# Kernel optimization log

Measured on AMD Instinct MI355X. Metric: run time of the kernel, lower is better.

## Reference

```python
import jax, jax.numpy as jnp
import numpy as np

N_NODES = 50000
N_EDGES = 600000
EMB_DIM = 128
HIDDEN = 128
BN_EPS = 1e-5


def setup_inputs() -> dict:
    key = jax.random.key(0)
    ks = jax.random.split(key, 8)
    s_in = 1.0 / np.sqrt(EMB_DIM)
    s_h = 1.0 / np.sqrt(HIDDEN)
    return {
        "x_idx": jnp.arange(N_NODES, dtype=jnp.int32),
        "edge_index": jax.random.randint(ks[0], (2, N_EDGES), 0, N_NODES, dtype=jnp.int32),
        "emb_table": jax.random.normal(ks[1], (N_NODES, EMB_DIM), jnp.float32),
        # ClusterGCNConv: lin_out (bias=False) and lin_root (bias=False)
        "W_out": jax.random.uniform(ks[2], (HIDDEN, EMB_DIM), jnp.float32, -s_in, s_in),
        "W_root": jax.random.uniform(ks[3], (HIDDEN, EMB_DIM), jnp.float32, -s_in, s_in),
        "bn0_gamma": jnp.ones((HIDDEN,), jnp.float32),
        "bn0_beta": jnp.zeros((HIDDEN,), jnp.float32),
        # SGConv 1 (K=1, add_self_loops=True, Linear with bias)
        "W_sg1": jax.random.uniform(ks[4], (HIDDEN, HIDDEN), jnp.float32, -s_h, s_h),
        "b_sg1": jnp.zeros((HIDDEN,), jnp.float32),
        "bn1_gamma": jnp.ones((HIDDEN,), jnp.float32),
        "bn1_beta": jnp.zeros((HIDDEN,), jnp.float32),
        # SGConv 2 (final layer)
        "W_sg2": jax.random.uniform(ks[5], (HIDDEN, HIDDEN), jnp.float32, -s_h, s_h),
        "b_sg2": jnp.zeros((HIDDEN,), jnp.float32),
    }


def _cluster_gcn(x, row, col, W_out, W_root, n):
    # PyG ClusterGCNConv (add_self_loops=False, diag_lambda=0, bias=False):
    # out[c] = sum_{(r->c)} (1/deg(c)) * x[r];  return out @ W_out^T + x @ W_root^T
    deg = jax.ops.segment_sum(jnp.ones_like(col, dtype=x.dtype), col, num_segments=n)
    deg_inv = 1.0 / jnp.maximum(deg, 1.0)
    msg = x[row] * deg_inv[col][:, None]                  # [E, D]
    agg = jax.ops.segment_sum(msg, col, num_segments=n)   # [N, D]
    return agg @ W_out.T + x @ W_root.T


def _sg_conv(x, row, col, W, b, n):
    # PyG SGConv K=1 with gcn_norm: A_hat = D^{-1/2}(A+I)D^{-1/2}, then Linear.
    loop = jnp.arange(n, dtype=row.dtype)
    r = jnp.concatenate([row, loop])
    c = jnp.concatenate([col, loop])
    deg = jax.ops.segment_sum(jnp.ones_like(c, dtype=x.dtype), c, num_segments=n)
    dis = jnp.where(deg > 0, jax.lax.rsqrt(jnp.maximum(deg, 1e-12)), 0.0)
    ew = dis[r] * dis[c]                                   # [E+N]
    agg = jax.ops.segment_sum(x[r] * ew[:, None], c, num_segments=n)
    return agg @ W.T + b


def _bn(x, gamma, beta):
    # BatchNorm1d in training mode: batch statistics, biased variance.
    mu = x.mean(axis=0)
    var = ((x - mu) ** 2).mean(axis=0)
    return (x - mu) * jax.lax.rsqrt(var + BN_EPS) * gamma + beta


def reference(x_idx, edge_index, emb_table, W_out, W_root, bn0_gamma, bn0_beta,
              W_sg1, b_sg1, bn1_gamma, bn1_beta, W_sg2, b_sg2):
    n = emb_table.shape[0]
    row, col = edge_index[0], edge_index[1]
    x = emb_table[x_idx]                                   # [N, D]
    # layer 0: ClusterGCNConv -> BN -> ReLU (dropout p=0)
    x = _cluster_gcn(x, row, col, W_out, W_root, n)
    x = jax.nn.relu(_bn(x, bn0_gamma, bn0_beta))
    # layer 1: SGConv -> BN -> ReLU
    x = _sg_conv(x, row, col, W_sg1, b_sg1, n)
    x = jax.nn.relu(_bn(x, bn1_gamma, bn1_beta))
    # final SGConv
    return _sg_conv(x, row, col, W_sg2, b_sg2, n)
```

## Files before the change

### kernel.cpp

```cpp
#include <hip/hip_runtime.h>
#include <stdint.h>

#define NN 50000
#define NE 600000
#define DD 128
#define BN_EPS 1e-5f

typedef __attribute__((ext_vector_type(8))) short short8;
typedef __attribute__((ext_vector_type(4))) float f32x4;

__device__ __forceinline__ float bf2f(uint16_t u) {
    union { uint32_t u; float f; } v; v.u = ((uint32_t)u) << 16; return v.f;
}
__device__ __forceinline__ uint16_t f2bf(float f) {
    union { float f; uint32_t u; } v; v.f = f;
    return (uint16_t)((v.u + 0x7FFFu + ((v.u >> 16) & 1u)) >> 16);
}
__device__ __forceinline__ float lo16(uint32_t v) { return bf2f((uint16_t)(v & 0xFFFFu)); }
__device__ __forceinline__ float hi16(uint32_t v) { return bf2f((uint16_t)(v >> 16)); }

__global__ void k_count(const int* __restrict__ col, int* __restrict__ cnt) {
    int e = blockIdx.x * 256 + threadIdx.x;
    if (e < NE) atomicAdd(&cnt[col[e]], 1);
}

__global__ void k_alloc(const int* __restrict__ cnt, int* __restrict__ cursor,
                        int* __restrict__ off, int* __restrict__ fillp,
                        float* __restrict__ deginv, float* __restrict__ dis,
                        int* __restrict__ csr_row) {
    int i = blockIdx.x * 256 + threadIdx.x;
    if (i >= NN) return;
    int deg = cnt[i];
    int padded = (deg + 7) & ~7;
    int base = atomicAdd(cursor, padded);
    off[i] = base;
    fillp[i] = base;
    deginv[i] = 1.0f / fmaxf((float)deg, 1.0f);
    dis[i] = rsqrtf((float)deg + 1.0f);
    for (int p = deg; p < padded; ++p) csr_row[base + p] = NN;
}

__global__ void k_fill(const int* __restrict__ ei, int* __restrict__ fillp,
                       int* __restrict__ csr_row) {
    int e = blockIdx.x * 256 + threadIdx.x;
    if (e < NE) {
        int c = ei[NE + e];
        int p = atomicAdd(&fillp[c], 1);
        csr_row[p] = ei[e];
    }
}

__global__ void k_gather(const int* __restrict__ x_idx, const float* __restrict__ emb,
                         uint16_t* __restrict__ xb) {
    int idx = blockIdx.x * 256 + threadIdx.x;
    if (idx >= (NN + 1) * 32) return;
    int node = idx >> 5, c4 = (idx & 31) << 2;
    ushort4 o;
    if (node == NN) {
        o.x = 0; o.y = 0; o.z = 0; o.w = 0;
    } else {
        int src = x_idx[node];
        float4 v = *(const float4*)(emb + (size_t)src * DD + c4);
        o.x = f2bf(v.x); o.y = f2bf(v.y); o.z = f2bf(v.z); o.w = f2bf(v.w);
    }
    *(ushort4*)(xb + (size_t)node * DD + c4) = o;
}

template<int MODE>
__global__ __launch_bounds__(256)
void k_agg(const uint16_t* __restrict__ xb, const int* __restrict__ off,
           const int* __restrict__ cnt, const int* __restrict__ csr_row,
           const float* __restrict__ deginv, const float* __restrict__ dis,
           uint16_t* __restrict__ aggb) {
    int node = blockIdx.x * 4 + (threadIdx.x >> 6);
    if (node >= NN) return;
    int lane = threadIdx.x & 63;
    const uint32_t* __restrict__ xw = (const uint32_t*)xb;
    float a0 = 0.0f, a1 = 0.0f;
    if (MODE == 1) {
        uint32_t v = xw[(size_t)node * 64 + lane];
        a0 = lo16(v); a1 = hi16(v);
    }
    int s = off[node];
    int padded = (cnt[node] + 7) & ~7;
    for (int base = 0; base < padded; base += 64) {
        int rem = min(padded - base, 64);
        int idxv = (lane < rem) ? csr_row[s + base + lane] : NN;
        for (int i = 0; i < rem; i += 8) {
            uint32_t v[8];
            #pragma unroll
            for (int u = 0; u < 8; ++u) {
                int r = __builtin_amdgcn_readlane(idxv, i + u);
                v[u] = xw[(size_t)r * 64 + lane];
            }
            #pragma unroll
            for (int u = 0; u < 8; ++u) { a0 += lo16(v[u]); a1 += hi16(v[u]); }
        }
    }
    float sc = (MODE == 1) ? dis[node] : deginv[node];
    a0 *= sc; a1 *= sc;
    uint32_t o = (uint32_t)f2bf(a0) | ((uint32_t)f2bf(a1) << 16);
    *(uint32_t*)(aggb + (size_t)node * DD + lane * 2) = o;
}

template<bool DUAL, bool STATS, bool BIAS, bool STORE_BF16>
__global__ __launch_bounds__(256, 2)
void k_gemm(const uint16_t* __restrict__ A1, const uint16_t* __restrict__ A2,
            const float* __restrict__ W1, const float* __restrict__ W2,
            const float* __restrict__ bias, float* __restrict__ Hf,
            uint16_t* __restrict__ Hb, float* __restrict__ stats) {
    __shared__ uint16_t Alds[128 * 128];
    __shared__ uint16_t Wlds[128 * 128];
    const int t = threadIdx.x;
    const int lane = t & 63, wid = t >> 6;
    const int wm = (wid >> 1) * 64, wn = (wid & 1) * 64;
    const int m0 = blockIdx.x * 128;
    f32x4 zero = {0.0f, 0.0f, 0.0f, 0.0f};
    f32x4 acc[4][4];
    #pragma unroll
    for (int m = 0; m < 4; ++m)
        #pragma unroll
        for (int n = 0; n < 4; ++n) acc[m][n] = zero;

    const int NP = DUAL ? 2 : 1;
    for (int p = 0; p < NP; ++p) {
        const uint16_t* A = (DUAL && p) ? A2 : A1;
        const float* W = (DUAL && p) ? W2 : W1;
        if (p) __syncthreads();
        #pragma unroll
        for (int it = 0; it < 8; ++it) {
            int idx = it * 256 + t;
            int row = idx >> 4, c16 = idx & 15;
            uint32_t boff = (uint32_t)(row * 256 + ((c16 * 16) ^ ((row & 7) << 4)));
            uint4 v = make_uint4(0u, 0u, 0u, 0u);
            if (m0 + row < NN)
                v = *(const uint4*)(A + (size_t)(m0 + row) * DD + c16 * 8);
            *(uint4*)((char*)Alds + boff) = v;
        }
        #pragma unroll
        for (int it = 0; it < 8; ++it) {
            int idx = it * 256 + t;
            int row = idx >> 4, c8 = idx & 15;
            const float* wp = W + row * DD + c8 * 8;
            float4 v0 = *(const float4*)(wp);
            float4 v1 = *(const float4*)(wp + 4);
            uint4 pk;
            pk.x = (uint32_t)f2bf(v0.x) | ((uint32_t)f2bf(v0.y) << 16);
            pk.y = (uint32_t)f2bf(v0.z) | ((uint32_t)f2bf(v0.w) << 16);
            pk.z = (uint32_t)f2bf(v1.x) | ((uint32_t)f2bf(v1.y) << 16);
            pk.w = (uint32_t)f2bf(v1.z) | ((uint32_t)f2bf(v1.w) << 16);
            uint32_t boff = (uint32_t)(row * 256 + ((c8 * 16) ^ ((row & 7) << 4)));
            *(uint4*)((char*)Wlds + boff) = pk;
        }
        __syncthreads();
        #pragma unroll
        for (int ks = 0; ks < 4; ++ks) {
            short8 a[4], b[4];
            int kb = ks * 64 + ((lane >> 4) << 4);
            #pragma unroll
            for (int m = 0; m < 4; ++m) {
                int row = wm + m * 16 + (lane & 15);
                a[m] = *(const short8*)((const char*)Alds + row * 256 + (kb ^ ((row & 7) << 4)));
            }
            #pragma unroll
            for (int n = 0; n < 4; ++n) {
                int row = wn + n * 16 + (lane & 15);
                b[n] = *(const short8*)((const char*)Wlds + row * 256 + (kb ^ ((row & 7) << 4)));
            }
            #pragma unroll
            for (int m = 0; m < 4; ++m)
                #pragma unroll
                for (int n = 0; n < 4; ++n)
                    acc[m][n] = __builtin_amdgcn_mfma_f32_16x16x32_bf16(a[m], b[n], acc[m][n], 0, 0, 0);
        }
    }
    #pragma unroll
    for (int n = 0; n < 4; ++n) {
        int col = wn + n * 16 + (lane & 15);
        float bb = BIAS ? bias[col] : 0.0f;
        float ssum = 0.0f, ssq = 0.0f;
        #pragma unroll
        for (int m = 0; m < 4; ++m) {
            int rbase = m0 + wm + m * 16 + ((lane >> 4) << 2);
            #pragma unroll
            for (int i = 0; i < 4; ++i) {
                int gr = rbase + i;
                if (gr < NN) {
                    float v = acc[m][n][i] + bb;
                    if (STORE_BF16) Hb[(size_t)gr * DD + col] = f2bf(v);
                    else            Hf[(size_t)gr * DD + col] = v;
                    ssum += v; ssq += v * v;
                }
            }
        }
        if (STATS) {
            ssum += __shfl_xor(ssum, 16, 64);
            ssum += __shfl_xor(ssum, 32, 64);
            ssq  += __shfl_xor(ssq, 16, 64);
            ssq  += __shfl_xor(ssq, 32, 64);
            if (lane < 16) {
                atomicAdd(&stats[col], ssum);
                atomicAdd(&stats[DD + col], ssq);
            }
        }
    }
}

__global__ __launch_bounds__(256)
void k_bnrelu(const uint16_t* __restrict__ Hb, const float* __restrict__ st,
              const float* __restrict__ gamma, const float* __restrict__ beta,
              const float* __restrict__ dis, uint16_t* __restrict__ xb) {
    __shared__ float s_sc[128], s_of[128];
    int t = threadIdx.x;
    if (t < 128) {
        const float invn = 1.0f / (float)NN;
        float mean = st[t] * invn;
        float var = st[DD + t] * invn - mean * mean;
        float sc = gamma[t] * rsqrtf(var + BN_EPS);
        s_sc[t] = sc;
        s_of[t] = beta[t] - mean * sc;
    }
    __syncthreads();
    int idx = blockIdx.x * 256 + t;
    int node = idx >> 4, c8 = (idx & 15) << 3;
    if (node >= NN) return;
    float d = dis[node];
    uint4 h = *(const uint4*)(Hb + (size_t)node * DD + c8);
    uint32_t hw[4] = {h.x, h.y, h.z, h.w};
    uint32_t ow[4];
    #pragma unroll
    for (int j = 0; j < 4; ++j) {
        int c = c8 + j * 2;
        float v0 = fmaxf(lo16(hw[j]) * s_sc[c]     + s_of[c],     0.0f) * d;
        float v1 = fmaxf(hi16(hw[j]) * s_sc[c + 1] + s_of[c + 1], 0.0f) * d;
        ow[j] = (uint32_t)f2bf(v0) | ((uint32_t)f2bf(v1) << 16);
    }
    uint4 o = make_uint4(ow[0], ow[1], ow[2], ow[3]);
    *(uint4*)(xb + (size_t)node * DD + c8) = o;
}

extern "C" void kernel_launch(void* const* d_in, const int* in_sizes, int n_in,
                              void* d_out, int out_size, void* d_ws, size_t ws_size,
                              hipStream_t stream) {
    const int* x_idx   = (const int*)d_in[0];
    const int* ei      = (const int*)d_in[1];
    const float* emb   = (const float*)d_in[2];
    const float* W_out = (const float*)d_in[3];
    const float* W_root= (const float*)d_in[4];
    const float* g0    = (const float*)d_in[5];
    const float* be0   = (const float*)d_in[6];
    const float* W1    = (const float*)d_in[7];
    const float* b1    = (const float*)d_in[8];
    const float* g1    = (const float*)d_in[9];
    const float* be1   = (const float*)d_in[10];
    const float* W2    = (const float*)d_in[11];
    const float* b2    = (const float*)d_in[12];
    float* out = (float*)d_out;

    char* ws = (char*)d_ws;
    size_t o = 0;
    auto carve = [&](size_t bytes) -> void* {
        void* p = ws + o;
        o = (o + bytes + 255) & ~(size_t)255;
        return p;
    };
    int* cnt      = (int*)carve((size_t)NN * 4);
    int* cursor   = (int*)carve(4);
    float* st0    = (float*)carve(256 * 4);
    float* st1    = (float*)carve(256 * 4);
    size_t zlen = o;
    int* fillp    = (int*)carve((size_t)NN * 4);
    int* off      = (int*)carve((size_t)NN * 4);
    float* deginv = (float*)carve((size_t)NN * 4);
    float* dis    = (float*)carve((size_t)NN * 4);
    int* csr_row  = (int*)carve((size_t)(NE + NN * 8) * 4);
    uint16_t* xb  = (uint16_t*)carve((size_t)(NN + 1) * DD * 2);
    uint16_t* aggb= (uint16_t*)carve((size_t)NN * DD * 2);
    uint16_t* hb  = (uint16_t*)carve((size_t)NN * DD * 2);

    hipMemsetAsync(ws, 0, zlen, stream);

    const int EB = (NE + 255) / 256;
    const int NB = (NN + 255) / 256;
    const int GB = (NN + 127) / 128;
    const int AB = (NN + 3) / 4;
    const int VB = ((NN + 1) * 32 + 255) / 256;
    const int BB = (NN * 16 + 255) / 256;

    k_count<<<EB, 256, 0, stream>>>(ei + NE, cnt);
    k_alloc<<<NB, 256, 0, stream>>>(cnt, cursor, off, fillp, deginv, dis, csr_row);
    k_fill<<<EB, 256, 0, stream>>>(ei, fillp, csr_row);
    k_gather<<<VB, 256, 0, stream>>>(x_idx, emb, xb);

    k_agg<0><<<AB, 256, 0, stream>>>(xb, off, cnt, csr_row, deginv, dis, aggb);
    k_gemm<true, true, false, true><<<GB, 256, 0, stream>>>(
        aggb, xb, W_out, W_root, nullptr, nullptr, hb, st0);
    k_bnrelu<<<BB, 256, 0, stream>>>(hb, st0, g0, be0, dis, xb);

    k_agg<1><<<AB, 256, 0, stream>>>(xb, off, cnt, csr_row, deginv, dis, aggb);
    k_gemm<false, true, true, true><<<GB, 256, 0, stream>>>(
        aggb, nullptr, W1, nullptr, b1, nullptr, hb, st1);
    k_bnrelu<<<BB, 256, 0, stream>>>(hb, st1, g1, be1, dis, xb);

    k_agg<1><<<AB, 256, 0, stream>>>(xb, off, cnt, csr_row, deginv, dis, aggb);
    k_gemm<false, false, true, false><<<GB, 256, 0, stream>>>(
        aggb, nullptr, W2, nullptr, b2, out, nullptr, nullptr);
}
```

Before: 266.1 us.

## Drop CSR padding, use wave prefix-scan allocation, and replace memset with kernel

The CSR build no longer pads each node's neighbour list to a multiple of 8 with a dummy zero row. Offsets are now allocated by a wavefront prefix scan, with one atomic per wave instead of one per node. The aggregation kernel handles the leftover neighbours with 4-wide and scalar tail loops, which removes the wasted gathers of the dummy row. A small zeroing kernel replaces hipMemsetAsync, so the tail loops add some control overhead in exchange.

New measurement: 268.7 us. No clear change (+1.0%).

```diff
diff --git a/kernel.cpp b/kernel.cpp
--- a/kernel.cpp
+++ b/kernel.cpp
@@ -19,6 +19,11 @@
 __device__ __forceinline__ float lo16(uint32_t v) { return bf2f((uint16_t)(v & 0xFFFFu)); }
 __device__ __forceinline__ float hi16(uint32_t v) { return bf2f((uint16_t)(v >> 16)); }
 
+__global__ void k_zero(uint4* __restrict__ p, int n16) {
+    int i = blockIdx.x * 256 + threadIdx.x;
+    if (i < n16) p[i] = make_uint4(0u, 0u, 0u, 0u);
+}
+
 __global__ void k_count(const int* __restrict__ col, int* __restrict__ cnt) {
     int e = blockIdx.x * 256 + threadIdx.x;
     if (e < NE) atomicAdd(&cnt[col[e]], 1);
@@ -26,18 +31,27 @@
 
 __global__ void k_alloc(const int* __restrict__ cnt, int* __restrict__ cursor,
                         int* __restrict__ off, int* __restrict__ fillp,
-                        float* __restrict__ deginv, float* __restrict__ dis,
-                        int* __restrict__ csr_row) {
+                        float* __restrict__ deginv, float* __restrict__ dis) {
     int i = blockIdx.x * 256 + threadIdx.x;
-    if (i >= NN) return;
-    int deg = cnt[i];
-    int padded = (deg + 7) & ~7;
-    int base = atomicAdd(cursor, padded);
-    off[i] = base;
-    fillp[i] = base;
-    deginv[i] = 1.0f / fmaxf((float)deg, 1.0f);
-    dis[i] = rsqrtf((float)deg + 1.0f);
-    for (int p = deg; p < padded; ++p) csr_row[base + p] = NN;
+    int lane = threadIdx.x & 63;
+    int deg = (i < NN) ? cnt[i] : 0;
+    int v = deg;
+    #pragma unroll
+    for (int d = 1; d < 64; d <<= 1) {
+        int t = __shfl_up(v, d, 64);
+        if (lane >= d) v += t;
+    }
+    int total = __shfl(v, 63, 64);
+    int wbase = 0;
+    if (lane == 63) wbase = atomicAdd(cursor, total);
+    wbase = __shfl(wbase, 63, 64);
+    int base = wbase + v - deg;
+    if (i < NN) {
+        off[i] = base;
+        fillp[i] = base;
+        deginv[i] = 1.0f / fmaxf((float)deg, 1.0f);
+        dis[i] = rsqrtf((float)deg + 1.0f);
+    }
 }
 
 __global__ void k_fill(const int* __restrict__ ei, int* __restrict__ fillp,
@@ -53,16 +67,12 @@
 __global__ void k_gather(const int* __restrict__ x_idx, const float* __restrict__ emb,
                          uint16_t* __restrict__ xb) {
     int idx = blockIdx.x * 256 + threadIdx.x;
-    if (idx >= (NN + 1) * 32) return;
+    if (idx >= NN * 32) return;
     int node = idx >> 5, c4 = (idx & 31) << 2;
+    int src = x_idx[node];
+    float4 v = *(const float4*)(emb + (size_t)src * DD + c4);
     ushort4 o;
-    if (node == NN) {
-        o.x = 0; o.y = 0; o.z = 0; o.w = 0;
-    } else {
-        int src = x_idx[node];
-        float4 v = *(const float4*)(emb + (size_t)src * DD + c4);
-        o.x = f2bf(v.x); o.y = f2bf(v.y); o.z = f2bf(v.z); o.w = f2bf(v.w);
-    }
+    o.x = f2bf(v.x); o.y = f2bf(v.y); o.z = f2bf(v.z); o.w = f2bf(v.w);
     *(ushort4*)(xb + (size_t)node * DD + c4) = o;
 }
 
@@ -81,12 +91,12 @@
         uint32_t v = xw[(size_t)node * 64 + lane];
         a0 = lo16(v); a1 = hi16(v);
     }
-    int s = off[node];
-    int padded = (cnt[node] + 7) & ~7;
-    for (int base = 0; base < padded; base += 64) {
-        int rem = min(padded - base, 64);
-        int idxv = (lane < rem) ? csr_row[s + base + lane] : NN;
-        for (int i = 0; i < rem; i += 8) {
+    int s = off[node], e = s + cnt[node];
+    for (int base = s; base < e; base += 64) {
+        int c64 = min(e - base, 64);
+        int idxv = (lane < c64) ? csr_row[base + lane] : 0;
+        int i = 0;
+        for (; i + 8 <= c64; i += 8) {
             uint32_t v[8];
             #pragma unroll
             for (int u = 0; u < 8; ++u) {
@@ -95,6 +105,22 @@
             }
             #pragma unroll
             for (int u = 0; u < 8; ++u) { a0 += lo16(v[u]); a1 += hi16(v[u]); }
+        }
+        if (i + 4 <= c64) {
+            uint32_t v[4];
+            #pragma unroll
+            for (int u = 0; u < 4; ++u) {
+                int r = __builtin_amdgcn_readlane(idxv, i + u);
+                v[u] = xw[(size_t)r * 64 + lane];
+            }
+            #pragma unroll
+            for (int u = 0; u < 4; ++u) { a0 += lo16(v[u]); a1 += hi16(v[u]); }
+            i += 4;
+        }
+        for (; i < c64; ++i) {
+            int r = __builtin_amdgcn_readlane(idxv, i);
+            uint32_t v = xw[(size_t)r * 64 + lane];
+            a0 += lo16(v); a1 += hi16(v);
         }
     }
     float sc = (MODE == 1) ? dis[node] : deginv[node];
@@ -273,22 +299,22 @@
     int* off      = (int*)carve((size_t)NN * 4);
     float* deginv = (float*)carve((size_t)NN * 4);
     float* dis    = (float*)carve((size_t)NN * 4);
-    int* csr_row  = (int*)carve((size_t)(NE + NN * 8) * 4);
-    uint16_t* xb  = (uint16_t*)carve((size_t)(NN + 1) * DD * 2);
+    int* csr_row  = (int*)carve((size_t)NE * 4);
+    uint16_t* xb  = (uint16_t*)carve((size_t)NN * DD * 2);
     uint16_t* aggb= (uint16_t*)carve((size_t)NN * DD * 2);
     uint16_t* hb  = (uint16_t*)carve((size_t)NN * DD * 2);
 
-    hipMemsetAsync(ws, 0, zlen, stream);
-
+    const int ZB = (int)((zlen / 16 + 255) / 256);
     const int EB = (NE + 255) / 256;
     const int NB = (NN + 255) / 256;
     const int GB = (NN + 127) / 128;
     const int AB = (NN + 3) / 4;
-    const int VB = ((NN + 1) * 32 + 255) / 256;
+    const int VB = (NN * 32 + 255) / 256;
     const int BB = (NN * 16 + 255) / 256;
 
+    k_zero<<<ZB, 256, 0, stream>>>((uint4*)ws, (int)(zlen / 16));
     k_count<<<EB, 256, 0, stream>>>(ei + NE, cnt);
-    k_alloc<<<NB, 256, 0, stream>>>(cnt, cursor, off, fillp, deginv, dis, csr_row);
+    k_alloc<<<NB, 256, 0, stream>>>(cnt, cursor, off, fillp, deginv, dis);
     k_fill<<<EB, 256, 0, stream>>>(ei, fillp, csr_row);
     k_gather<<<VB, 256, 0, stream>>>(x_idx, emb, xb);
 
```
